# Kernel optimization log

Measured on AMD Instinct MI355X. Metric: run time of the kernel, lower is better.

The kernel has to match this reference:

```python
import jax, jax.numpy as jnp
import numpy as np

B, P, DE, DD, DA = 256, 196, 2048, 512, 512

def setup_inputs() -> dict:
    key = jax.random.key(0)
    ks = jax.random.split(key, 8)
    s_enc = 1.0 / np.sqrt(DE)
    s_dec = 1.0 / np.sqrt(DD)
    s_att = 1.0 / np.sqrt(DA)
    return {
        "encoder_out": jax.random.normal(ks[0], (B, P, DE), dtype=jnp.float32),
        "decoder_hidden": jax.random.normal(ks[1], (B, DD), dtype=jnp.float32),
        "W_enc": jax.random.uniform(ks[2], (DE, DA), jnp.float32, -s_enc, s_enc),
        "b_enc": jax.random.uniform(ks[3], (DA,), jnp.float32, -s_enc, s_enc),
        "W_dec": jax.random.uniform(ks[4], (DD, DA), jnp.float32, -s_dec, s_dec),
        "b_dec": jax.random.uniform(ks[5], (DA,), jnp.float32, -s_dec, s_dec),
        "W_full": jax.random.uniform(ks[6], (DA, 1), jnp.float32, -s_att, s_att),
        "b_full": jax.random.uniform(ks[7], (1,), jnp.float32, -s_att, s_att),
    }

def reference(encoder_out, decoder_hidden, W_enc, b_enc, W_dec, b_dec, W_full, b_full):
    # att1: [B,P,DA]; att2: [B,DA]
    att1 = jnp.einsum('bpe,ea->bpa', encoder_out, W_enc) + b_enc
    att2 = decoder_hidden @ W_dec + b_dec
    # broadcast add + relu + project to scalar score per position
    att = jnp.einsum('bpa,a->bp', jax.nn.relu(att1 + att2[:, None, :]), W_full[:, 0]) + b_full[0]
    alpha = jax.nn.softmax(att, axis=1)  # [B,P]
    context_vector = jnp.einsum('bpe,bp->be', encoder_out, alpha)  # [B,DE]
    return (context_vector, alpha)
```

## Files before the change

### kernel.cpp

```cpp
#include <hip/hip_runtime.h>
#include <hip/hip_bf16.h>
#include <cstddef>

#define B_   256
#define P_   196
#define DE_  2048
#define DD_  512
#define DA_  512
#define M_   (B_*P_)

#define BM   112
#define KT   32

typedef __attribute__((ext_vector_type(4))) float f32x4;
typedef __attribute__((ext_vector_type(8))) short s16x8;

static __device__ __forceinline__ short f2bf(float x) {
    __hip_bfloat16 h = __float2bfloat16(x);
    return *reinterpret_cast<short*>(&h);
}

#define GLOAD_LDS16(g, l) __builtin_amdgcn_global_load_lds( \
    (const __attribute__((address_space(1))) void*)(g),     \
    (__attribute__((address_space(3))) void*)(l), 16, 0, 0)

__global__ void pack_wenc(const float* __restrict__ W, __hip_bfloat16* __restrict__ out) {
    __shared__ float lds[KT][128 + 1];
    const int kt = blockIdx.x;
    const int n0 = blockIdx.y * 128;
    const int t  = threadIdx.x;
#pragma unroll
    for (int i = 0; i < 16; ++i) {
        int e  = t + i * 256;
        int kl = e >> 7;
        int nl = e & 127;
        lds[kl][nl] = W[(size_t)(kt * KT + kl) * DA_ + n0 + nl];
    }
    __syncthreads();
    short* o16 = reinterpret_cast<short*>(out);
#pragma unroll
    for (int i = 0; i < 2; ++i) {
        int task = t + i * 256;
        int nl   = task >> 2;
        int s    = task & 3;
        int n    = n0 + nl;
        int sp   = s ^ ((n >> 1) & 3);
        s16x8 w;
#pragma unroll
        for (int j = 0; j < 8; ++j)
            w[j] = f2bf(lds[s * 8 + j][nl]);
        *reinterpret_cast<s16x8*>(o16 + (size_t)kt * (DA_ * KT) + n * KT + sp * 8) = w;
    }
}

__global__ __launch_bounds__(512) void att2_kernel(
        const float* __restrict__ dh, const float* __restrict__ W_dec,
        const float* __restrict__ b_dec, const float* __restrict__ b_enc,
        float* __restrict__ att2p) {
    __shared__ float s_dh[DD_];
    const int b = blockIdx.x;
    const int a = threadIdx.x;
    s_dh[a] = dh[(size_t)b * DD_ + a];
    __syncthreads();
    float acc = 0.f;
#pragma unroll 8
    for (int k = 0; k < DD_; ++k)
        acc += s_dh[k] * W_dec[(size_t)k * DA_ + a];
    att2p[(size_t)b * DA_ + a] = acc + b_dec[a] + b_enc[a];
}

__global__ __launch_bounds__(512, 2) void gemm_att(
        const float* __restrict__ enc, const __hip_bfloat16* __restrict__ Bp,
        const float* __restrict__ att2p, const float* __restrict__ Wfull,
        const float* __restrict__ bfull, float* __restrict__ att) {
    __shared__ __hip_bfloat16 a_lds[BM * KT];
    __shared__ __hip_bfloat16 b_lds[DA_ * KT];
    __shared__ float red[BM][8];

    const int tid  = threadIdx.x;
    const int wave = tid >> 6;
    const int lane = tid & 63;
    const int g    = lane >> 4;
    const int c    = lane & 15;
    const int block_row = blockIdx.x * BM;
    const int nbase = wave * 64;

    const int slot8 = (g ^ ((c >> 1) & 3)) * 8;

    const int ar = tid >> 2;
    const int aq = tid & 3;
    const bool a_active = (tid < BM * 4);
    __hip_bfloat16* a_dst = a_lds + ar * KT + (aq ^ ((ar >> 1) & 3)) * 8;
    const float* a_src = enc + (size_t)(block_row + ar) * DE_ + aq * 8;

    f32x4 acc[7][4] = {};

    for (int kt = 0; kt < DE_ / KT; ++kt) {
        __syncthreads();
        {
            const char* bsrc = (const char*)Bp + (size_t)kt * (DA_ * KT * 2) + (size_t)tid * 16;
            char*       bdst = (char*)b_lds + wave * 1024;
#pragma unroll
            for (int i = 0; i < 4; ++i)
                GLOAD_LDS16(bsrc + i * 8192, bdst + i * 8192);
        }
        if (a_active) {
            f32x4 v0 = *reinterpret_cast<const f32x4*>(a_src + kt * KT);
            f32x4 v1 = *reinterpret_cast<const f32x4*>(a_src + kt * KT + 4);
            s16x8 w;
            w[0] = f2bf(v0.x); w[1] = f2bf(v0.y); w[2] = f2bf(v0.z); w[3] = f2bf(v0.w);
            w[4] = f2bf(v1.x); w[5] = f2bf(v1.y); w[6] = f2bf(v1.z); w[7] = f2bf(v1.w);
            *reinterpret_cast<s16x8*>(a_dst) = w;
        }
        __syncthreads();
        s16x8 afrag[7], bfrag[4];
#pragma unroll
        for (int mt = 0; mt < 7; ++mt)
            afrag[mt] = *reinterpret_cast<const s16x8*>(a_lds + (mt * 16 + c) * KT + slot8);
#pragma unroll
        for (int nt = 0; nt < 4; ++nt)
            bfrag[nt] = *reinterpret_cast<const s16x8*>(b_lds + (nbase + nt * 16 + c) * KT + slot8);
#pragma unroll
        for (int mt = 0; mt < 7; ++mt)
#pragma unroll
            for (int nt = 0; nt < 4; ++nt)
                acc[mt][nt] = __builtin_amdgcn_mfma_f32_16x16x32_bf16(
                                  afrag[mt], bfrag[nt], acc[mt][nt], 0, 0, 0);
    }

    const int b0    = block_row / P_;
    const int b1    = min(b0 + 1, B_ - 1);
    const int split = (b0 + 1) * P_;
    float wf[4], a20[4], a21[4];
#pragma unroll
    for (int nt = 0; nt < 4; ++nt) {
        const int n = nbase + nt * 16 + c;
        wf[nt]  = Wfull[n];
        a20[nt] = att2p[(size_t)b0 * DA_ + n];
        a21[nt] = att2p[(size_t)b1 * DA_ + n];
    }
#pragma unroll
    for (int mt = 0; mt < 7; ++mt) {
#pragma unroll
        for (int q = 0; q < 4; ++q) {
            const int row_local = mt * 16 + g * 4 + q;
            const int R = block_row + row_local;
            const bool hi = (R >= split);
            float s = 0.f;
#pragma unroll
            for (int nt = 0; nt < 4; ++nt) {
                float a2 = hi ? a21[nt] : a20[nt];
                float v  = acc[mt][nt][q] + a2;
                v = fmaxf(v, 0.f);
                s += v * wf[nt];
            }
#pragma unroll
            for (int off = 1; off < 16; off <<= 1)
                s += __shfl_xor(s, off, 64);
            if (c == 0) red[row_local][wave] = s;
        }
    }
    __syncthreads();
    if (tid < BM) {
        float t = 0.f;
#pragma unroll
        for (int w = 0; w < 8; ++w) t += red[tid][w];
        att[block_row + tid] = t + bfull[0];
    }
}

__global__ __launch_bounds__(256) void softmax_kernel(
        const float* __restrict__ att, float* __restrict__ alpha) {
    const int b = blockIdx.x;
    const int t = threadIdx.x;
    __shared__ float sred[4];
    float v = (t < P_) ? att[(size_t)b * P_ + t] : -1e30f;
    float m = v;
#pragma unroll
    for (int off = 1; off < 64; off <<= 1) m = fmaxf(m, __shfl_xor(m, off, 64));
    if ((t & 63) == 0) sred[t >> 6] = m;
    __syncthreads();
    const float mall = fmaxf(fmaxf(sred[0], sred[1]), fmaxf(sred[2], sred[3]));
    __syncthreads();
    float e = (t < P_) ? expf(v - mall) : 0.f;
    float s = e;
#pragma unroll
    for (int off = 1; off < 64; off <<= 1) s += __shfl_xor(s, off, 64);
    if ((t & 63) == 0) sred[t >> 6] = s;
    __syncthreads();
    const float stot = sred[0] + sred[1] + sred[2] + sred[3];
    if (t < P_) alpha[(size_t)b * P_ + t] = e / stot;
}

__global__ __launch_bounds__(256) void context_kernel(
        const float* __restrict__ enc, const float* __restrict__ alpha,
        float* __restrict__ ctx) {
    const int b = blockIdx.x;
    const int e = blockIdx.y * 1024 + threadIdx.x * 4;
    __shared__ float s_alpha[P_];
    if (threadIdx.x < P_) s_alpha[threadIdx.x] = alpha[(size_t)b * P_ + threadIdx.x];
    __syncthreads();
    f32x4 acc = {0.f, 0.f, 0.f, 0.f};
    const float* base = enc + (size_t)b * P_ * DE_ + e;
#pragma unroll 4
    for (int p = 0; p < P_; ++p) {
        f32x4 v = *reinterpret_cast<const f32x4*>(base + (size_t)p * DE_);
        acc += s_alpha[p] * v;
    }
    *reinterpret_cast<f32x4*>(ctx + (size_t)b * DE_ + e) = acc;
}

extern "C" void kernel_launch(void* const* d_in, const int* in_sizes, int n_in,
                              void* d_out, int out_size, void* d_ws, size_t ws_size,
                              hipStream_t stream) {
    const float* enc    = (const float*)d_in[0];
    const float* dh     = (const float*)d_in[1];
    const float* W_enc  = (const float*)d_in[2];
    const float* b_enc  = (const float*)d_in[3];
    const float* W_dec  = (const float*)d_in[4];
    const float* b_dec  = (const float*)d_in[5];
    const float* W_full = (const float*)d_in[6];
    const float* b_full = (const float*)d_in[7];

    float* out       = (float*)d_out;
    float* ctx_out   = out;
    float* alpha_out = out + (size_t)B_ * DE_;

    char* ws = (char*)d_ws;
    __hip_bfloat16* Bp = (__hip_bfloat16*)ws;
    float* att2p = (float*)(ws + 2u * 1024 * 1024);
    float* att   = (float*)(ws + 2u * 1024 * 1024 + 512u * 1024);

    pack_wenc   <<<dim3(64, 4),     256, 0, stream>>>(W_enc, Bp);
    att2_kernel <<<B_,              512, 0, stream>>>(dh, W_dec, b_dec, b_enc, att2p);
    gemm_att    <<<M_ / BM,         512, 0, stream>>>(enc, Bp, att2p, W_full, b_full, att);
    softmax_kernel<<<B_,            256, 0, stream>>>(att, alpha_out);
    context_kernel<<<dim3(B_, 2),   256, 0, stream>>>(enc, alpha_out, ctx_out);
}
```

Baseline: 312.1 us.

## Double-buffer LDS in attention GEMM with prefetched A tiles and manual waitcnt

The main bf16 MFMA GEMM now ping-pongs between two LDS buffers for both A and B. The next B tile is issued via global_load_lds and the A tile after that is prefetched into registers, both while the current tile's MFMAs run. This leaves one barrier per k-step instead of two, with explicit s_waitcnt to overlap global loads with compute. Doubling LDS use drops occupancy to one block of 512 threads per CU. It also adds manual vmcnt accounting and a dead ITER macro, so correctness depends on the hand-set wait counts.

```diff
diff --git a/kernel.cpp b/kernel.cpp
--- a/kernel.cpp
+++ b/kernel.cpp
@@ -11,6 +11,8 @@
 
 #define BM   112
 #define KT   32
+#define NKT  (DE_/KT)
+#define AROWS 128
 
 typedef __attribute__((ext_vector_type(4))) float f32x4;
 typedef __attribute__((ext_vector_type(8))) short s16x8;
@@ -69,12 +71,14 @@
     att2p[(size_t)b * DA_ + a] = acc + b_dec[a] + b_enc[a];
 }
 
-__global__ __launch_bounds__(512, 2) void gemm_att(
+__global__ __launch_bounds__(512, 1) void gemm_att(
         const float* __restrict__ enc, const __hip_bfloat16* __restrict__ Bp,
         const float* __restrict__ att2p, const float* __restrict__ Wfull,
         const float* __restrict__ bfull, float* __restrict__ att) {
-    __shared__ __hip_bfloat16 a_lds[BM * KT];
-    __shared__ __hip_bfloat16 b_lds[DA_ * KT];
+    __shared__ __hip_bfloat16 a_lds0[AROWS * KT];
+    __shared__ __hip_bfloat16 a_lds1[AROWS * KT];
+    __shared__ __hip_bfloat16 b_lds0[DA_ * KT];
+    __shared__ __hip_bfloat16 b_lds1[DA_ * KT];
     __shared__ float red[BM][8];
 
     const int tid  = threadIdx.x;
@@ -84,49 +88,99 @@
     const int c    = lane & 15;
     const int block_row = blockIdx.x * BM;
     const int nbase = wave * 64;
-
     const int slot8 = (g ^ ((c >> 1) & 3)) * 8;
 
-    const int ar = tid >> 2;
-    const int aq = tid & 3;
-    const bool a_active = (tid < BM * 4);
-    __hip_bfloat16* a_dst = a_lds + ar * KT + (aq ^ ((ar >> 1) & 3)) * 8;
-    const float* a_src = enc + (size_t)(block_row + ar) * DE_ + aq * 8;
+    const int ar   = tid >> 2;
+    const int aq   = tid & 3;
+    const int lrow = (ar < BM) ? ar : (ar & 15);
+    const int a_woff = ar * KT + (aq ^ ((ar >> 1) & 3)) * 8;
+    const float* ap = enc + (size_t)(block_row + lrow) * DE_ + aq * 8;
 
     f32x4 acc[7][4] = {};
-
-    for (int kt = 0; kt < DE_ / KT; ++kt) {
-        __syncthreads();
-        {
-            const char* bsrc = (const char*)Bp + (size_t)kt * (DA_ * KT * 2) + (size_t)tid * 16;
-            char*       bdst = (char*)b_lds + wave * 1024;
-#pragma unroll
-            for (int i = 0; i < 4; ++i)
-                GLOAD_LDS16(bsrc + i * 8192, bdst + i * 8192);
-        }
-        if (a_active) {
-            f32x4 v0 = *reinterpret_cast<const f32x4*>(a_src + kt * KT);
-            f32x4 v1 = *reinterpret_cast<const f32x4*>(a_src + kt * KT + 4);
-            s16x8 w;
-            w[0] = f2bf(v0.x); w[1] = f2bf(v0.y); w[2] = f2bf(v0.z); w[3] = f2bf(v0.w);
-            w[4] = f2bf(v1.x); w[5] = f2bf(v1.y); w[6] = f2bf(v1.z); w[7] = f2bf(v1.w);
-            *reinterpret_cast<s16x8*>(a_dst) = w;
-        }
-        __syncthreads();
-        s16x8 afrag[7], bfrag[4];
-#pragma unroll
-        for (int mt = 0; mt < 7; ++mt)
-            afrag[mt] = *reinterpret_cast<const s16x8*>(a_lds + (mt * 16 + c) * KT + slot8);
-#pragma unroll
-        for (int nt = 0; nt < 4; ++nt)
-            bfrag[nt] = *reinterpret_cast<const s16x8*>(b_lds + (nbase + nt * 16 + c) * KT + slot8);
-#pragma unroll
-        for (int mt = 0; mt < 7; ++mt)
-#pragma unroll
-            for (int nt = 0; nt < 4; ++nt)
-                acc[mt][nt] = __builtin_amdgcn_mfma_f32_16x16x32_bf16(
-                                  afrag[mt], bfrag[nt], acc[mt][nt], 0, 0, 0);
-    }
+    f32x4 pa0, pa1, pb0, pb1;
+
+#define STORE_A(dstbase, v0, v1) do {                                   \
+        s16x8 w_;                                                       \
+        w_[0]=f2bf((v0).x); w_[1]=f2bf((v0).y); w_[2]=f2bf((v0).z); w_[3]=f2bf((v0).w); \
+        w_[4]=f2bf((v1).x); w_[5]=f2bf((v1).y); w_[6]=f2bf((v1).z); w_[7]=f2bf((v1).w); \
+        *reinterpret_cast<s16x8*>((dstbase) + a_woff) = w_;             \
+    } while (0)
+
+#define ISSUE_B(T, dstb) do {                                           \
+        const char* bs_ = (const char*)Bp + (size_t)(T) * (DA_*KT*2) + (size_t)tid * 16; \
+        char* bd_ = (char*)(dstb) + (size_t)tid * 16;                   \
+        GLOAD_LDS16(bs_,           bd_);                                \
+        GLOAD_LDS16(bs_ +  8192,   bd_ +  8192);                        \
+        GLOAD_LDS16(bs_ + 16384,   bd_ + 16384);                        \
+        GLOAD_LDS16(bs_ + 24576,   bd_ + 24576);                        \
+    } while (0)
+
+#define FRAGS_MFMA(abuf, bbuf) do {                                     \
+        s16x8 af[7], bf[4];                                             \
+        _Pragma("unroll")                                               \
+        for (int mt = 0; mt < 7; ++mt)                                  \
+            af[mt] = *reinterpret_cast<const s16x8*>((abuf) + (mt*16 + c) * KT + slot8); \
+        _Pragma("unroll")                                               \
+        for (int nt = 0; nt < 4; ++nt)                                  \
+            bf[nt] = *reinterpret_cast<const s16x8*>((bbuf) + (nbase + nt*16 + c) * KT + slot8); \
+        _Pragma("unroll")                                               \
+        for (int mt = 0; mt < 7; ++mt)                                  \
+            _Pragma("unroll")                                           \
+            for (int nt = 0; nt < 4; ++nt)                              \
+                acc[mt][nt] = __builtin_amdgcn_mfma_f32_16x16x32_bf16(  \
+                                  af[mt], bf[nt], acc[mt][nt], 0, 0, 0);\
+    } while (0)
+
+#define FENCE_AFTER_BARRIER() do {                                      \
+        asm volatile("" ::: "memory");                                  \
+        __builtin_amdgcn_sched_barrier(0);                              \
+    } while (0)
+
+    pa0 = *reinterpret_cast<const f32x4*>(ap);
+    pa1 = *reinterpret_cast<const f32x4*>(ap + 4);
+    ISSUE_B(0, b_lds0);
+    pb0 = *reinterpret_cast<const f32x4*>(ap + KT);
+    pb1 = *reinterpret_cast<const f32x4*>(ap + KT + 4);
+    STORE_A(a_lds0, pa0, pa1);
+    asm volatile("s_waitcnt vmcnt(2) lgkmcnt(0)" ::: "memory");
+    __builtin_amdgcn_s_barrier();
+    FENCE_AFTER_BARRIER();
+
+#define ITER(T, ACUR, BCUR, ANXT, BNXT, C0, C1, I0, I1) do {            \
+        ISSUE_B((T)+1, BNXT);                                           \
+        I0 = *reinterpret_cast<const f32x4*>(ap + ((T)+2 - (T)/2*2) * 0 + 0); \
+        (void)0;                                                        \
+    } while (0)
+#undef ITER
+
+    const float* ap_it = ap;
+#pragma clang loop unroll(disable)
+    for (int kt = 0; kt < 62; kt += 2) {
+        ISSUE_B(kt + 1, b_lds1);
+        pa0 = *reinterpret_cast<const f32x4*>(ap_it + 2 * KT);
+        pa1 = *reinterpret_cast<const f32x4*>(ap_it + 2 * KT + 4);
+        FRAGS_MFMA(a_lds0, b_lds0);
+        STORE_A(a_lds1, pb0, pb1);
+        asm volatile("s_waitcnt vmcnt(2) lgkmcnt(0)" ::: "memory");
+        __builtin_amdgcn_s_barrier();
+        FENCE_AFTER_BARRIER();
+        ISSUE_B(kt + 2, b_lds0);
+        pb0 = *reinterpret_cast<const f32x4*>(ap_it + 3 * KT);
+        pb1 = *reinterpret_cast<const f32x4*>(ap_it + 3 * KT + 4);
+        FRAGS_MFMA(a_lds1, b_lds1);
+        STORE_A(a_lds0, pa0, pa1);
+        asm volatile("s_waitcnt vmcnt(2) lgkmcnt(0)" ::: "memory");
+        __builtin_amdgcn_s_barrier();
+        FENCE_AFTER_BARRIER();
+        ap_it += 2 * KT;
+    }
+    ISSUE_B(63, b_lds1);
+    FRAGS_MFMA(a_lds0, b_lds0);
+    STORE_A(a_lds1, pb0, pb1);
+    asm volatile("s_waitcnt vmcnt(0) lgkmcnt(0)" ::: "memory");
+    __builtin_amdgcn_s_barrier();
+    FENCE_AFTER_BARRIER();
+    FRAGS_MFMA(a_lds1, b_lds1);
 
     const int b0    = block_row / P_;
     const int b1    = min(b0 + 1, B_ - 1);
@@ -167,6 +221,10 @@
         for (int w = 0; w < 8; ++w) t += red[tid][w];
         att[block_row + tid] = t + bfull[0];
     }
+#undef STORE_A
+#undef ISSUE_B
+#undef FRAGS_MFMA
+#undef FENCE_AFTER_BARRIER
 }
 
 __global__ __launch_bounds__(256) void softmax_kernel(
```

Result: faster. 274.9 us (-11.9%).

## Split attention GEMM into N-panels with direct fp32 LDS loads and partial scores

Applied to the files above, without the earlier changes.

The fused GEMM now uses 128x128 tiles with 4 waves per 256-thread block and splits the 512-wide attention dimension into four panels. A grouped block order is meant to keep each encoder tile in L2 while its four panels run. Encoder rows are copied as fp32 straight into LDS with async global-to-LDS loads and converted to bf16 per wave, instead of being converted by threads before the LDS write. Each panel writes a partial score, and the softmax kernel sums the four partials. The softmax-invariant scalar bias is dropped. The cost is that the encoder is read and converted four times, relying on cache reuse to stay cheap.

```diff
diff --git a/kernel.cpp b/kernel.cpp
--- a/kernel.cpp
+++ b/kernel.cpp
@@ -9,8 +9,9 @@
 #define DA_  512
 #define M_   (B_*P_)
 
-#define BM   112
+#define BM   128
 #define KT   32
+#define NKT  (DE_/KT)
 
 typedef __attribute__((ext_vector_type(4))) float f32x4;
 typedef __attribute__((ext_vector_type(8))) short s16x8;
@@ -69,63 +70,73 @@
     att2p[(size_t)b * DA_ + a] = acc + b_dec[a] + b_enc[a];
 }
 
-__global__ __launch_bounds__(512, 2) void gemm_att(
+__global__ __launch_bounds__(256, 2) void gemm_att(
         const float* __restrict__ enc, const __hip_bfloat16* __restrict__ Bp,
         const float* __restrict__ att2p, const float* __restrict__ Wfull,
-        const float* __restrict__ bfull, float* __restrict__ att) {
-    __shared__ __hip_bfloat16 a_lds[BM * KT];
-    __shared__ __hip_bfloat16 b_lds[DA_ * KT];
-    __shared__ float red[BM][8];
+        float* __restrict__ att_part) {
+    __shared__ float a_lds[BM * KT];
+    __shared__ __hip_bfloat16 b_lds[128 * KT];
+    __shared__ float red[BM][2];
 
     const int tid  = threadIdx.x;
     const int wave = tid >> 6;
     const int lane = tid & 63;
     const int g    = lane >> 4;
     const int c    = lane & 15;
-    const int block_row = blockIdx.x * BM;
-    const int nbase = wave * 64;
-
-    const int slot8 = (g ^ ((c >> 1) & 3)) * 8;
-
-    const int ar = tid >> 2;
-    const int aq = tid & 3;
-    const bool a_active = (tid < BM * 4);
-    __hip_bfloat16* a_dst = a_lds + ar * KT + (aq ^ ((ar >> 1) & 3)) * 8;
-    const float* a_src = enc + (size_t)(block_row + ar) * DE_ + aq * 8;
-
-    f32x4 acc[7][4] = {};
-
-    for (int kt = 0; kt < DE_ / KT; ++kt) {
+    const int wm   = wave >> 1;
+    const int wn   = wave & 1;
+
+    const int p     = blockIdx.x;
+    const int q     = p >> 5;
+    const int t5    = p & 31;
+    const int panel = t5 >> 3;
+    const int mtile = q * 8 + (t5 & 7);
+    const int block_row = mtile * BM;
+
+    const int a_sslot = (tid & 7) ^ ((tid >> 3) & 7);
+    const float* a_src0 = enc + (size_t)(block_row + (tid >> 3)) * DE_ + a_sslot * 4;
+
+    const char* b_src0 = (const char*)Bp + (size_t)panel * 8192 + (size_t)tid * 16;
+
+    const int ax = c & 7;
+    const int ao0 = (((2 * g)     ^ ax)) * 4;
+    const int ao1 = (((2 * g + 1) ^ ax)) * 4;
+    const int bslot8 = (g ^ ((c >> 1) & 3)) * 8;
+
+    f32x4 acc[4][4] = {};
+
+    for (int kt = 0; kt < NKT; ++kt) {
         __syncthreads();
-        {
-            const char* bsrc = (const char*)Bp + (size_t)kt * (DA_ * KT * 2) + (size_t)tid * 16;
-            char*       bdst = (char*)b_lds + wave * 1024;
-#pragma unroll
-            for (int i = 0; i < 4; ++i)
-                GLOAD_LDS16(bsrc + i * 8192, bdst + i * 8192);
-        }
-        if (a_active) {
-            f32x4 v0 = *reinterpret_cast<const f32x4*>(a_src + kt * KT);
-            f32x4 v1 = *reinterpret_cast<const f32x4*>(a_src + kt * KT + 4);
+#pragma unroll
+        for (int i = 0; i < 4; ++i)
+            GLOAD_LDS16(a_src0 + (size_t)i * 32 * DE_ + kt * KT,
+                        &a_lds[(i * 256 + tid) * 4]);
+#pragma unroll
+        for (int i = 0; i < 2; ++i)
+            GLOAD_LDS16(b_src0 + (size_t)kt * 32768 + i * 4096,
+                        &b_lds[(i * 256 + tid) * 8]);
+        __syncthreads();
+        s16x8 af[4], bf[4];
+#pragma unroll
+        for (int mt = 0; mt < 4; ++mt) {
+            const float* base = a_lds + (wm * 64 + mt * 16 + c) * KT;
+            f32x4 v0 = *reinterpret_cast<const f32x4*>(base + ao0);
+            f32x4 v1 = *reinterpret_cast<const f32x4*>(base + ao1);
             s16x8 w;
             w[0] = f2bf(v0.x); w[1] = f2bf(v0.y); w[2] = f2bf(v0.z); w[3] = f2bf(v0.w);
             w[4] = f2bf(v1.x); w[5] = f2bf(v1.y); w[6] = f2bf(v1.z); w[7] = f2bf(v1.w);
-            *reinterpret_cast<s16x8*>(a_dst) = w;
+            af[mt] = w;
         }
-        __syncthreads();
-        s16x8 afrag[7], bfrag[4];
-#pragma unroll
-        for (int mt = 0; mt < 7; ++mt)
-            afrag[mt] = *reinterpret_cast<const s16x8*>(a_lds + (mt * 16 + c) * KT + slot8);
 #pragma unroll
         for (int nt = 0; nt < 4; ++nt)
-            bfrag[nt] = *reinterpret_cast<const s16x8*>(b_lds + (nbase + nt * 16 + c) * KT + slot8);
-#pragma unroll
-        for (int mt = 0; mt < 7; ++mt)
+            bf[nt] = *reinterpret_cast<const s16x8*>(
+                         b_lds + (wn * 64 + nt * 16 + c) * KT + bslot8);
+#pragma unroll
+        for (int mt = 0; mt < 4; ++mt)
 #pragma unroll
             for (int nt = 0; nt < 4; ++nt)
                 acc[mt][nt] = __builtin_amdgcn_mfma_f32_16x16x32_bf16(
-                                  afrag[mt], bfrag[nt], acc[mt][nt], 0, 0, 0);
+                                  af[mt], bf[nt], acc[mt][nt], 0, 0, 0);
     }
 
     const int b0    = block_row / P_;
@@ -134,47 +145,47 @@
     float wf[4], a20[4], a21[4];
 #pragma unroll
     for (int nt = 0; nt < 4; ++nt) {
-        const int n = nbase + nt * 16 + c;
-        wf[nt]  = Wfull[n];
-        a20[nt] = att2p[(size_t)b0 * DA_ + n];
-        a21[nt] = att2p[(size_t)b1 * DA_ + n];
-    }
-#pragma unroll
-    for (int mt = 0; mt < 7; ++mt) {
-#pragma unroll
-        for (int q = 0; q < 4; ++q) {
-            const int row_local = mt * 16 + g * 4 + q;
+        const int col = panel * 128 + wn * 64 + nt * 16 + c;
+        wf[nt]  = Wfull[col];
+        a20[nt] = att2p[(size_t)b0 * DA_ + col];
+        a21[nt] = att2p[(size_t)b1 * DA_ + col];
+    }
+#pragma unroll
+    for (int mt = 0; mt < 4; ++mt) {
+#pragma unroll
+        for (int qq = 0; qq < 4; ++qq) {
+            const int row_local = wm * 64 + mt * 16 + g * 4 + qq;
             const int R = block_row + row_local;
-            const bool hi = (R >= split);
+            const bool hiB = (R >= split);
             float s = 0.f;
 #pragma unroll
             for (int nt = 0; nt < 4; ++nt) {
-                float a2 = hi ? a21[nt] : a20[nt];
-                float v  = acc[mt][nt][q] + a2;
+                float a2 = hiB ? a21[nt] : a20[nt];
+                float v  = acc[mt][nt][qq] + a2;
                 v = fmaxf(v, 0.f);
                 s += v * wf[nt];
             }
 #pragma unroll
             for (int off = 1; off < 16; off <<= 1)
                 s += __shfl_xor(s, off, 64);
-            if (c == 0) red[row_local][wave] = s;
+            if (c == 0) red[row_local][wn] = s;
         }
     }
     __syncthreads();
-    if (tid < BM) {
-        float t = 0.f;
-#pragma unroll
-        for (int w = 0; w < 8; ++w) t += red[tid][w];
-        att[block_row + tid] = t + bfull[0];
-    }
+    if (tid < BM)
+        att_part[(size_t)panel * M_ + block_row + tid] = red[tid][0] + red[tid][1];
 }
 
 __global__ __launch_bounds__(256) void softmax_kernel(
-        const float* __restrict__ att, float* __restrict__ alpha) {
+        const float* __restrict__ att_part, float* __restrict__ alpha) {
     const int b = blockIdx.x;
     const int t = threadIdx.x;
     __shared__ float sred[4];
-    float v = (t < P_) ? att[(size_t)b * P_ + t] : -1e30f;
+    float v = -1e30f;
+    if (t < P_) {
+        const size_t R = (size_t)b * P_ + t;
+        v = att_part[R] + att_part[M_ + R] + att_part[2 * M_ + R] + att_part[3 * M_ + R];
+    }
     float m = v;
 #pragma unroll
     for (int off = 1; off < 64; off <<= 1) m = fmaxf(m, __shfl_xor(m, off, 64));
@@ -220,20 +231,19 @@
     const float* W_dec  = (const float*)d_in[4];
     const float* b_dec  = (const float*)d_in[5];
     const float* W_full = (const float*)d_in[6];
-    const float* b_full = (const float*)d_in[7];
 
     float* out       = (float*)d_out;
     float* ctx_out   = out;
     float* alpha_out = out + (size_t)B_ * DE_;
 
     char* ws = (char*)d_ws;
-    __hip_bfloat16* Bp = (__hip_bfloat16*)ws;
-    float* att2p = (float*)(ws + 2u * 1024 * 1024);
-    float* att   = (float*)(ws + 2u * 1024 * 1024 + 512u * 1024);
-
-    pack_wenc   <<<dim3(64, 4),     256, 0, stream>>>(W_enc, Bp);
-    att2_kernel <<<B_,              512, 0, stream>>>(dh, W_dec, b_dec, b_enc, att2p);
-    gemm_att    <<<M_ / BM,         512, 0, stream>>>(enc, Bp, att2p, W_full, b_full, att);
-    softmax_kernel<<<B_,            256, 0, stream>>>(att, alpha_out);
-    context_kernel<<<dim3(B_, 2),   256, 0, stream>>>(enc, alpha_out, ctx_out);
-}
+    __hip_bfloat16* Bp  = (__hip_bfloat16*)ws;
+    float* att2p    = (float*)(ws + 2u * 1024 * 1024);
+    float* att_part = (float*)(ws + 2u * 1024 * 1024 + 512u * 1024);
+
+    pack_wenc     <<<dim3(NKT, 4),   256, 0, stream>>>(W_enc, Bp);
+    att2_kernel   <<<B_,             512, 0, stream>>>(dh, W_dec, b_dec, b_enc, att2p);
+    gemm_att      <<<(M_ / BM) * 4,  256, 0, stream>>>(enc, Bp, att2p, W_full, att_part);
+    softmax_kernel<<<B_,             256, 0, stream>>>(att_part, alpha_out);
+    context_kernel<<<dim3(B_, 2),    256, 0, stream>>>(enc, alpha_out, ctx_out);
+}
```

Result: faster. 280.9 us (-10.0%).
